# Kernel optimization log

Measured on AMD Instinct MI355X. Metric: run time of the kernel, lower is better.

## Reference

```python
import jax, jax.numpy as jnp
import numpy as np

B, K, T, C, F = 2048, 32, 365, 4, 128  # batch, prototypes, steps, bands, feature_size


def conv1d(x, w, b, pad):
    # x: (B, Cin, T), w: (Cout, Cin, Kw)
    y = jax.lax.conv_general_dilated(x, w, (1,), [(pad, pad)],
                                     dimension_numbers=('NCH', 'OIH', 'NCH'))
    return y + b[None, :, None]


def bn_relu(x, gamma, beta):
    # training-mode BatchNorm1d over (batch, time) per channel
    mu = x.mean((0, 2), keepdims=True)
    var = x.var((0, 2), keepdims=True)
    xn = (x - mu) * jax.lax.rsqrt(var + 1e-5)
    return jax.nn.relu(xn * gamma[None, :, None] + beta[None, :, None])


def encoder(x, w1, b1, g1, be1, w2, b2, g2, be2, w3, b3, g3, be3, fc_w, fc_b):
    # FCNBaseline: 3 conv blocks + global average pool + linear
    h = x.transpose(0, 2, 1)                    # (B, C, T)
    h = bn_relu(conv1d(h, w1, b1, 4), g1, be1)  # (B, 128, T+1)
    h = bn_relu(conv1d(h, w2, b2, 2), g2, be2)  # (B, 256, *)
    h = bn_relu(conv1d(h, w3, b3, 1), g3, be3)  # (B, 128, *)
    return h.mean(-1) @ fc_w.T + fc_b           # (B, F)


def setup_inputs() -> dict:
    key = jax.random.key(0)
    ks = jax.random.split(key, 12)
    input_seq = jax.random.normal(ks[0], (B, T, C), jnp.float32)
    label = jax.random.randint(ks[1], (B,), 0, 9)
    mask = (jax.random.uniform(ks[2], (B, T)) > 0.2).astype(jnp.float32)
    prototypes = jax.random.normal(ks[3], (K, T, C), jnp.float32)
    w1 = jax.random.normal(ks[4], (128, C, 8)) * 0.05
    b1 = jnp.zeros((128,)); g1 = jnp.ones((128,)); be1 = jnp.zeros((128,))
    w2 = jax.random.normal(ks[5], (256, 128, 5)) * 0.05
    b2 = jnp.zeros((256,)); g2 = jnp.ones((256,)); be2 = jnp.zeros((256,))
    w3 = jax.random.normal(ks[6], (128, 256, 3)) * 0.05
    b3 = jnp.zeros((128,)); g3 = jnp.ones((128,)); be3 = jnp.zeros((128,))
    fc_w = jax.random.normal(ks[7], (F, 128)) * 0.05
    fc_b = jnp.zeros((F,))
    off_w = jax.random.normal(ks[8], (K * C, F)) * 0.05
    off_b = jnp.zeros((K * C,))
    return dict(input_seq=input_seq, label=label, mask=mask, prototypes=prototypes,
                w1=w1, b1=b1, g1=g1, be1=be1, w2=w2, b2=b2, g2=g2, be2=be2,
                w3=w3, b3=b3, g3=g3, be3=be3, fc_w=fc_w, fc_b=fc_b,
                off_w=off_w, off_b=off_b)


def reference(input_seq, label, mask, prototypes, w1, b1, g1, be1, w2, b2, g2, be2,
              w3, b3, g3, be3, fc_w, fc_b, off_w, off_b):
    # trans_activ=False (TPS warp disabled), offset_activ=True, unsupervised path
    feat = encoder(input_seq, w1, b1, g1, be1, w2, b2, g2, be2, w3, b3, g3, be3, fc_w, fc_b)
    offset = jnp.tanh(feat @ off_w.T + off_b).reshape(-1, K, 1, C)  # (B,K,1,C)
    protos = prototypes[None] + offset                              # (B,K,T,C)
    diff = input_seq[:, None] - protos                              # (B,K,T,C)
    # masked squared-distance reduce: mask (B,T) broadcasts over (K,C)
    distances = jnp.einsum('bktc,bt->bk', diff * diff, mask)        # (B,K)
    indices = jnp.argmin(distances, axis=1)                         # (B,)
    output_seq = jnp.take_along_axis(protos, indices[:, None, None, None], axis=1)[:, 0]
    return output_seq
```

## Files before the change

### kernel.cpp

```cpp
#include <hip/hip_runtime.h>
#include <hip/hip_bf16.h>

#define BB 2048
#define TIN 365
#define TO 366
#define C1 128
#define C2 256
#define C3 128
#define FF 128

typedef __attribute__((ext_vector_type(4))) float f32x4v;
typedef __attribute__((ext_vector_type(8))) short bf16x8;

__device__ inline unsigned short f2bf(float v) {
  unsigned u = __float_as_uint(v);
  unsigned r = (u + 0x7FFF + ((u >> 16) & 1)) >> 16;
  return (unsigned short)r;
}
__device__ inline float bf2f(unsigned short b) {
  return __uint_as_float(((unsigned)b) << 16);
}

__global__ void wprep2_kernel(const float* __restrict__ w2,
                              short* __restrict__ wh, short* __restrict__ wl) {
  int n = 256 * 128 * 5;
  for (int idx = blockIdx.x * 256 + threadIdx.x; idx < n; idx += gridDim.x * 256) {
    int k = idx % 5;
    int rest = idx / 5;
    int i = rest % 128;
    int o = rest / 128;
    float v = w2[idx];
    unsigned short hb = f2bf(v);
    unsigned short lb = f2bf(v - bf2f(hb));
    size_t dst = ((((size_t)k * 4 + (i >> 5)) * 16 + (o >> 4)) * 64 +
                  ((i >> 3) & 3) * 16 + (o & 15)) * 8 + (i & 7);
    wh[dst] = (short)hb;
    wl[dst] = (short)lb;
  }
}
__global__ void wprep3_kernel(const float* __restrict__ w3,
                              short* __restrict__ wh, short* __restrict__ wl) {
  int n = 128 * 256 * 3;
  for (int idx = blockIdx.x * 256 + threadIdx.x; idx < n; idx += gridDim.x * 256) {
    int k = idx % 3;
    int rest = idx / 3;
    int i = rest % 256;
    int o = rest / 256;
    float v = w3[idx];
    unsigned short hb = f2bf(v);
    unsigned short lb = f2bf(v - bf2f(hb));
    size_t dst = ((((size_t)k * 8 + (i >> 5)) * 8 + (o >> 4)) * 64 +
                  ((i >> 3) & 3) * 16 + (o & 15)) * 8 + (i & 7);
    wh[dst] = (short)hb;
    wl[dst] = (short)lb;
  }
}

__global__ void bnparam_kernel(const double* __restrict__ sums,
                               const float* __restrict__ gamma,
                               const float* __restrict__ beta, int Cch,
                               float* __restrict__ scale, float* __restrict__ shift) {
  int i = threadIdx.x;
  if (i < Cch) {
    const double N = (double)BB * (double)TO;
    double mean = sums[i] / N;
    double var = sums[Cch + i] / N - mean * mean;
    double sc = (double)gamma[i] / sqrt(var + 1e-5);
    scale[i] = (float)sc;
    shift[i] = (float)((double)beta[i] - mean * sc);
  }
}

__global__ __launch_bounds__(256) void conv1_stats_kernel(
    const float* __restrict__ x, const float* __restrict__ w1,
    const float* __restrict__ b1, double* __restrict__ sums) {
  __shared__ float4 xs[374];
  __shared__ float ws1[4096];
  int tid = threadIdx.x;
  for (int i = tid; i < 4096; i += 256) ws1[i] = w1[i];
  __syncthreads();
  const int o = tid >> 1, half = tid & 1;
  float wr[32];
#pragma unroll
  for (int i = 0; i < 32; ++i) wr[i] = ws1[o * 32 + i];
  const float bo = b1[o];
  float s1 = 0.f, s2 = 0.f;
  for (int b = blockIdx.x * 8; b < blockIdx.x * 8 + 8; ++b) {
    __syncthreads();
    for (int u = tid; u < 374; u += 256) {
      int t_in = u - 4;
      float4 v = make_float4(0.f, 0.f, 0.f, 0.f);
      if (t_in >= 0 && t_in < TIN) v = *(const float4*)(x + ((size_t)b * TIN + t_in) * 4);
      xs[u] = v;
    }
    __syncthreads();
    for (int t = half * 183; t < half * 183 + 183; ++t) {
      float acc = bo;
#pragma unroll
      for (int k = 0; k < 8; ++k) {
        float4 xv = xs[t + k];
        acc = fmaf(wr[k], xv.x, acc);
        acc = fmaf(wr[8 + k], xv.y, acc);
        acc = fmaf(wr[16 + k], xv.z, acc);
        acc = fmaf(wr[24 + k], xv.w, acc);
      }
      s1 += acc; s2 += acc * acc;
    }
  }
  s1 += __shfl_xor(s1, 1);
  s2 += __shfl_xor(s2, 1);
  if (half == 0) {
    atomicAdd(&sums[o], (double)s1);
    atomicAdd(&sums[C1 + o], (double)s2);
  }
}

__global__ __launch_bounds__(256) void conv2_mfma_kernel(
    const float* __restrict__ x, const float* __restrict__ w1g,
    const float* __restrict__ b1, const float* __restrict__ scale1,
    const float* __restrict__ shift1, const short* __restrict__ w2ph,
    const short* __restrict__ w2pl, const float* __restrict__ b2,
    float* __restrict__ p2) {
  __shared__ float ws1[4096];
  __shared__ float4 xwin[76];
  __shared__ __align__(16) short h1h[68 * 72];
  __shared__ __align__(16) short h1l[68 * 72];
  __shared__ float sstat[512];
  const int tid = threadIdx.x;
  const int tt = blockIdx.x, b = blockIdx.y;
  const int tbase = tt * 64;
  const int slice = (b * 6 + tt) & 63;
  const int w = tid >> 6, lane = tid & 63;
  const int q = lane >> 4, l15 = lane & 15;

  for (int i = tid; i < 4096; i += 256) ws1[i] = w1g[i];
  for (int u = tid; u < 76; u += 256) {
    int tx = tbase - 6 + u;
    float4 v = make_float4(0.f, 0.f, 0.f, 0.f);
    if (tx >= 0 && tx < TIN) v = *(const float4*)(x + ((size_t)b * TIN + tx) * 4);
    xwin[u] = v;
  }
  float b2r[4][4];
#pragma unroll
  for (int om = 0; om < 4; ++om)
#pragma unroll
    for (int r = 0; r < 4; ++r) b2r[om][r] = b2[64 * w + om * 16 + q * 4 + r];

  f32x4v acc[4][4];
#pragma unroll
  for (int om = 0; om < 4; ++om)
#pragma unroll
    for (int nt = 0; nt < 4; ++nt) acc[om][nt] = (f32x4v){0.f, 0.f, 0.f, 0.f};

  const int chl = tid >> 2, qt = tid & 3;
  for (int ic2 = 0; ic2 < 2; ++ic2) {
    __syncthreads();
    {
      int ch = ic2 * 64 + chl;
      float sc = scale1[ch], sh = shift1[ch], bo = b1[ch];
      const float* wr = &ws1[ch * 32];
      for (int j = 0; j < 17; ++j) {
        int u = qt * 17 + j;
        int t = tbase - 2 + u;
        float a = bo;
#pragma unroll
        for (int kk = 0; kk < 8; ++kk) {
          float4 xv = xwin[u + kk];
          a = fmaf(wr[kk], xv.x, a);
          a = fmaf(wr[8 + kk], xv.y, a);
          a = fmaf(wr[16 + kk], xv.z, a);
          a = fmaf(wr[24 + kk], xv.w, a);
        }
        float v = (t >= 0 && t < TO) ? fmaxf(fmaf(sc, a, sh), 0.f) : 0.f;
        unsigned short hb = f2bf(v);
        h1h[u * 72 + chl] = (short)hb;
        h1l[u * 72 + chl] = (short)f2bf(v - bf2f(hb));
      }
    }
    __syncthreads();
    for (int k = 0; k < 5; ++k) {
      for (int ic = 0; ic < 2; ++ic) {
        int icg = ic2 * 2 + ic;
        bf16x8 ah[4], al[4];
#pragma unroll
        for (int om = 0; om < 4; ++om) {
          int og = 4 * w + om;
          size_t base = ((((size_t)k * 4 + icg) * 16 + og) * 64 + lane) * 8;
          ah[om] = *(const bf16x8*)(w2ph + base);
          al[om] = *(const bf16x8*)(w2pl + base);
        }
        int ioff = ic * 32 + q * 8;
#pragma unroll
        for (int nt = 0; nt < 4; ++nt) {
          int u = nt * 16 + l15 + k;
          bf16x8 bh = *(const bf16x8*)&h1h[u * 72 + ioff];
          bf16x8 bl = *(const bf16x8*)&h1l[u * 72 + ioff];
#pragma unroll
          for (int om = 0; om < 4; ++om) {
            acc[om][nt] = __builtin_amdgcn_mfma_f32_16x16x32_bf16(ah[om], bh, acc[om][nt], 0, 0, 0);
            acc[om][nt] = __builtin_amdgcn_mfma_f32_16x16x32_bf16(ah[om], bl, acc[om][nt], 0, 0, 0);
            acc[om][nt] = __builtin_amdgcn_mfma_f32_16x16x32_bf16(al[om], bh, acc[om][nt], 0, 0, 0);
          }
        }
      }
    }
  }
  float ts1[16], ts2[16];
#pragma unroll
  for (int i = 0; i < 16; ++i) { ts1[i] = 0.f; ts2[i] = 0.f; }
#pragma unroll
  for (int om = 0; om < 4; ++om)
#pragma unroll
    for (int nt = 0; nt < 4; ++nt) {
      int t = tbase + nt * 16 + l15;
      if (t < TO) {
#pragma unroll
        for (int r = 0; r < 4; ++r) {
          float v = acc[om][nt][r] + b2r[om][r];
          ts1[om * 4 + r] += v;
          ts2[om * 4 + r] += v * v;
        }
      }
    }
#pragma unroll
  for (int i = 0; i < 16; ++i) {
#pragma unroll
    for (int d = 1; d < 16; d <<= 1) {
      ts1[i] += __shfl_xor(ts1[i], d);
      ts2[i] += __shfl_xor(ts2[i], d);
    }
  }
  if (l15 == 0) {
#pragma unroll
    for (int om = 0; om < 4; ++om)
#pragma unroll
      for (int r = 0; r < 4; ++r) {
        int o = 64 * w + om * 16 + q * 4 + r;
        sstat[o] = ts1[om * 4 + r];
        sstat[256 + o] = ts2[om * 4 + r];
      }
  }
  __syncthreads();
  atomicAdd(&p2[(size_t)tid * 64 + slice], sstat[tid]);
  atomicAdd(&p2[((size_t)tid + 256) * 64 + slice], sstat[tid + 256]);
}

template <int EPI>
__global__ __launch_bounds__(256) void fused23_kernel(
    const float* __restrict__ x, const float* __restrict__ w1g,
    const float* __restrict__ b1, const float* __restrict__ scale1,
    const float* __restrict__ shift1, const short* __restrict__ w2ph,
    const short* __restrict__ w2pl, const float* __restrict__ b2,
    const float* __restrict__ scale2, const float* __restrict__ shift2,
    const short* __restrict__ w3ph, const short* __restrict__ w3pl,
    const float* __restrict__ b3, const float* __restrict__ scale3,
    const float* __restrict__ shift3, float* __restrict__ p3,
    float* __restrict__ pooled, float* __restrict__ h3g,
    int bstore, int boff) {
  __shared__ float4 xwin[80];
  __shared__ __align__(16) short un[17424];
  __shared__ float bn2s[768];
  __shared__ float sstat[256];
  short* h1h = un;
  short* h1l = un + 70 * 72;
  short* h2sh = un;
  short* h2sl = un + 66 * 132;
  const int tid = threadIdx.x;
  const int tt = blockIdx.x;
  const int b = blockIdx.y + boff;
  const int tbase = tt * 64;
  const int slice = (b * 6 + tt) & 63;
  const int w = tid >> 6, lane = tid & 63;
  const int q = lane >> 4, l15 = lane & 15;

  for (int u = tid; u < 77; u += 256) {
    int tx = tbase - 7 + u;
    float4 v = make_float4(0.f, 0.f, 0.f, 0.f);
    if (tx >= 0 && tx < TIN) v = *(const float4*)(x + ((size_t)b * TIN + tx) * 4);
    xwin[u] = v;
  }
  bn2s[tid] = b2[tid];
  bn2s[256 + tid] = scale2[tid];
  bn2s[512 + tid] = shift2[tid];

  float b3r[2][4], sc3r[2][4], sh3r[2][4];
#pragma unroll
  for (int om = 0; om < 2; ++om)
#pragma unroll
    for (int r = 0; r < 4; ++r) {
      int o = 32 * w + om * 16 + q * 4 + r;
      b3r[om][r] = b3[o];
      if (EPI == 1) { sc3r[om][r] = scale3[o]; sh3r[om][r] = shift3[o]; }
    }

  f32x4v acc2[4][5];
#pragma unroll
  for (int om = 0; om < 4; ++om)
#pragma unroll
    for (int nt = 0; nt < 5; ++nt) acc2[om][nt] = (f32x4v){0.f, 0.f, 0.f, 0.f};

  const int chl = tid >> 2, qt = tid & 3;
  for (int ic2 = 0; ic2 < 2; ++ic2) {
    int ch = ic2 * 64 + chl;
    float wr[32];
#pragma unroll
    for (int i = 0; i < 32; ++i) wr[i] = w1g[ch * 32 + i];
    float sc = scale1[ch], sh = shift1[ch], bo = b1[ch];
    __syncthreads();
    for (int j = 0; j < 18; ++j) {
      int u1 = qt * 18 + j;
      if (u1 < 70) {
        int t1 = tbase - 3 + u1;
        float a = bo;
#pragma unroll
        for (int kk = 0; kk < 8; ++kk) {
          float4 xv = xwin[u1 + kk];
          a = fmaf(wr[kk], xv.x, a);
          a = fmaf(wr[8 + kk], xv.y, a);
          a = fmaf(wr[16 + kk], xv.z, a);
          a = fmaf(wr[24 + kk], xv.w, a);
        }
        float v = (t1 >= 0 && t1 < TO) ? fmaxf(fmaf(sc, a, sh), 0.f) : 0.f;
        unsigned short hb = f2bf(v);
        h1h[u1 * 72 + chl] = (short)hb;
        h1l[u1 * 72 + chl] = (short)f2bf(v - bf2f(hb));
      }
    }
    __syncthreads();
    for (int k = 0; k < 5; ++k) {
      for (int ic = 0; ic < 2; ++ic) {
        int icg = ic2 * 2 + ic;
        bf16x8 ah[4], al[4];
#pragma unroll
        for (int om = 0; om < 4; ++om) {
          int og = 4 * w + om;
          size_t base = ((((size_t)k * 4 + icg) * 16 + og) * 64 + lane) * 8;
          ah[om] = *(const bf16x8*)(w2ph + base);
          al[om] = *(const bf16x8*)(w2pl + base);
        }
        int ioff = ic * 32 + q * 8;
#pragma unroll
        for (int nt = 0; nt < 5; ++nt) {
          int u1 = nt * 16 + l15 + k;
          if (u1 > 69) u1 = 69;
          bf16x8 bh = *(const bf16x8*)&h1h[u1 * 72 + ioff];
          bf16x8 bl = *(const bf16x8*)&h1l[u1 * 72 + ioff];
#pragma unroll
          for (int om = 0; om < 4; ++om) {
            acc2[om][nt] = __builtin_amdgcn_mfma_f32_16x16x32_bf16(ah[om], bh, acc2[om][nt], 0, 0, 0);
            acc2[om][nt] = __builtin_amdgcn_mfma_f32_16x16x32_bf16(ah[om], bl, acc2[om][nt], 0, 0, 0);
            acc2[om][nt] = __builtin_amdgcn_mfma_f32_16x16x32_bf16(al[om], bh, acc2[om][nt], 0, 0, 0);
          }
        }
      }
    }
  }
  __syncthreads();
  f32x4v acc3[2][4];
#pragma unroll
  for (int om = 0; om < 2; ++om)
#pragma unroll
    for (int nt = 0; nt < 4; ++nt) acc3[om][nt] = (f32x4v){0.f, 0.f, 0.f, 0.f};
  for (int c = 0; c < 2; ++c) {
    if (c) __syncthreads();
#pragma unroll
    for (int ml = 0; ml < 2; ++ml) {
      int om = 2 * c + ml;
      int og = 4 * w + om;
#pragma unroll
      for (int nt = 0; nt < 5; ++nt) {
        int u2 = nt * 16 + l15;
        if (u2 < 66) {
          int t2 = tbase - 1 + u2;
          bool valid = (t2 >= 0 && t2 < TO);
#pragma unroll
          for (int rp = 0; rp < 2; ++rp) {
            int o = og * 16 + q * 4 + rp * 2;
            int ol = (w * 2 + ml) * 16 + q * 4 + rp * 2;
            float v0 = 0.f, v1 = 0.f;
            if (valid) {
              v0 = fmaxf(fmaf(bn2s[256 + o], acc2[om][nt][rp * 2] + bn2s[o], bn2s[512 + o]), 0.f);
              v1 = fmaxf(fmaf(bn2s[256 + o + 1], acc2[om][nt][rp * 2 + 1] + bn2s[o + 1], bn2s[512 + o + 1]), 0.f);
            }
            unsigned short hb0 = f2bf(v0), hb1 = f2bf(v1);
            *(unsigned*)&h2sh[u2 * 132 + ol] = (unsigned)hb0 | ((unsigned)hb1 << 16);
            *(unsigned*)&h2sl[u2 * 132 + ol] =
                (unsigned)f2bf(v0 - bf2f(hb0)) | ((unsigned)f2bf(v1 - bf2f(hb1)) << 16);
          }
        }
      }
    }
    __syncthreads();
    for (int k = 0; k < 3; ++k) {
      for (int e = 0; e < 4; ++e) {
        int icg = c + 2 * e;
        bf16x8 a3h[2], a3l[2];
#pragma unroll
        for (int om = 0; om < 2; ++om) {
          int og = 2 * w + om;
          size_t base = ((((size_t)k * 8 + icg) * 8 + og) * 64 + lane) * 8;
          a3h[om] = *(const bf16x8*)(w3ph + base);
          a3l[om] = *(const bf16x8*)(w3pl + base);
        }
        int ioff = e * 32 + q * 8;
#pragma unroll
        for (int nt = 0; nt < 4; ++nt) {
          int u = nt * 16 + l15 + k;
          bf16x8 bh = *(const bf16x8*)&h2sh[u * 132 + ioff];
          bf16x8 bl = *(const bf16x8*)&h2sl[u * 132 + ioff];
#pragma unroll
          for (int om = 0; om < 2; ++om) {
            acc3[om][nt] = __builtin_amdgcn_mfma_f32_16x16x32_bf16(a3h[om], bh, acc3[om][nt], 0, 0, 0);
            acc3[om][nt] = __builtin_amdgcn_mfma_f32_16x16x32_bf16(a3l[om], bh, acc3[om][nt], 0, 0, 0);
            acc3[om][nt] = __builtin_amdgcn_mfma_f32_16x16x32_bf16(a3h[om], bl, acc3[om][nt], 0, 0, 0);
          }
        }
      }
    }
  }
  if (EPI == 0) {
    float ts1[8], ts2[8];
#pragma unroll
    for (int i = 0; i < 8; ++i) { ts1[i] = 0.f; ts2[i] = 0.f; }
    bool st = (b < bstore);
#pragma unroll
    for (int om = 0; om < 2; ++om)
#pragma unroll
      for (int nt = 0; nt < 4; ++nt) {
        int t = tbase + nt * 16 + l15;
        if (t < TO) {
#pragma unroll
          for (int r = 0; r < 4; ++r) {
            float v = acc3[om][nt][r] + b3r[om][r];
            ts1[om * 4 + r] += v;
            ts2[om * 4 + r] += v * v;
            if (st) {
              int o = 32 * w + om * 16 + q * 4 + r;
              h3g[((size_t)b * 128 + o) * 368 + t] = v;
            }
          }
        }
      }
#pragma unroll
    for (int i = 0; i < 8; ++i) {
#pragma unroll
      for (int d = 1; d < 16; d <<= 1) {
        ts1[i] += __shfl_xor(ts1[i], d);
        ts2[i] += __shfl_xor(ts2[i], d);
      }
    }
    if (l15 == 0) {
#pragma unroll
      for (int om = 0; om < 2; ++om)
#pragma unroll
        for (int r = 0; r < 4; ++r) {
          int o = 32 * w + om * 16 + q * 4 + r;
          sstat[o] = ts1[om * 4 + r];
          sstat[128 + o] = ts2[om * 4 + r];
        }
    }
    __syncthreads();
    atomicAdd(&p3[(size_t)tid * 64 + slice], sstat[tid]);
  } else {
    float ps[8];
#pragma unroll
    for (int i = 0; i < 8; ++i) ps[i] = 0.f;
#pragma unroll
    for (int om = 0; om < 2; ++om)
#pragma unroll
      for (int nt = 0; nt < 4; ++nt) {
        int t = tbase + nt * 16 + l15;
        if (t < TO) {
#pragma unroll
          for (int r = 0; r < 4; ++r) {
            float v = acc3[om][nt][r] + b3r[om][r];
            ps[om * 4 + r] += fmaxf(fmaf(sc3r[om][r], v, sh3r[om][r]), 0.f);
          }
        }
      }
#pragma unroll
    for (int i = 0; i < 8; ++i) {
#pragma unroll
      for (int d = 1; d < 16; d <<= 1) ps[i] += __shfl_xor(ps[i], d);
    }
    if (l15 == 0) {
#pragma unroll
      for (int om = 0; om < 2; ++om)
#pragma unroll
        for (int r = 0; r < 4; ++r) {
          int o = 32 * w + om * 16 + q * 4 + r;
          atomicAdd(&pooled[(size_t)b * 128 + o], ps[om * 4 + r]);
        }
    }
  }
}

__global__ __launch_bounds__(256) void gap3_kernel(
    const float* __restrict__ h3g, const float* __restrict__ scale3,
    const float* __restrict__ shift3, float* __restrict__ pooled) {
  int b = blockIdx.x, tid = threadIdx.x;
  int w = tid >> 6, lane = tid & 63;
  for (int cc = 0; cc < 32; ++cc) {
    int ch = w * 32 + cc;
    float sc = scale3[ch], sh = shift3[ch];
    const float* row = h3g + ((size_t)b * 128 + ch) * 368;
    float s = 0.f;
    for (int u = lane; u < TO; u += 64)
      s += fmaxf(fmaf(sc, row[u], sh), 0.f);
#pragma unroll
    for (int d = 32; d > 0; d >>= 1) s += __shfl_xor(s, d);
    if (lane == 0) pooled[(size_t)b * 128 + ch] = s;
  }
}

__global__ __launch_bounds__(64) void reduce_slices_kernel(
    const float* __restrict__ p, double* __restrict__ sums) {
  int c = blockIdx.x, tid = threadIdx.x;
  double s = (double)p[(size_t)c * 64 + tid];
  for (int d = 32; d > 0; d >>= 1) s += __shfl_down(s, d);
  if (tid == 0) sums[c] = s;
}

__global__ __launch_bounds__(128) void head2_kernel(
    const float* __restrict__ pooled, const float* __restrict__ fc_w,
    const float* __restrict__ fc_b, const float* __restrict__ off_w,
    const float* __restrict__ off_b, float* __restrict__ offs) {
  int b = blockIdx.x, tid = threadIdx.x;
  __shared__ float pl[128], feat[128];
  pl[tid] = pooled[(size_t)b * C3 + tid] * (1.0f / 366.0f);
  __syncthreads();
  {
    const float* wr = fc_w + tid * FF;
    float a = fc_b[tid];
    for (int i = 0; i < 128; ++i) a = fmaf(pl[i], wr[i], a);
    feat[tid] = a;
  }
  __syncthreads();
  {
    const float* wr = off_w + tid * FF;
    float z = off_b[tid];
    for (int i = 0; i < 128; ++i) z = fmaf(feat[i], wr[i], z);
    offs[(size_t)b * 128 + tid] = tanhf(z);
  }
}

__global__ __launch_bounds__(256) void dist_kernel(
    const float* __restrict__ x, const float* __restrict__ mask,
    const float* __restrict__ protos, const float* __restrict__ offs,
    float* __restrict__ out) {
  int b = blockIdx.x, tid = threadIdx.x;
  __shared__ float ofl[128];
  __shared__ double dred[256];
  __shared__ int ksel;
  if (tid < 128) ofl[tid] = offs[(size_t)b * 128 + tid];
  __syncthreads();
  int k = tid & 31, tg = tid >> 5;
  float o0 = ofl[k * 4 + 0], o1 = ofl[k * 4 + 1], o2 = ofl[k * 4 + 2], o3 = ofl[k * 4 + 3];
  double acc = 0.0;
  for (int t = tg; t < TIN; t += 8) {
    float4 xv = *(const float4*)(x + ((size_t)b * TIN + t) * 4);
    float4 pv = *(const float4*)(protos + ((size_t)k * TIN + t) * 4);
    float m = mask[(size_t)b * TIN + t];
    float d0 = xv.x - pv.x - o0;
    float d1 = xv.y - pv.y - o1;
    float d2 = xv.z - pv.z - o2;
    float d3 = xv.w - pv.w - o3;
    acc += (double)(m * (d0 * d0 + d1 * d1 + d2 * d2 + d3 * d3));
  }
  dred[tid] = acc;
  __syncthreads();
  if (tid < 32) {
    double s = 0.0;
    for (int g = 0; g < 8; ++g) s += dred[g * 32 + tid];
    dred[tid] = s;
  }
  __syncthreads();
  if (tid == 0) {
    double best = dred[0]; int bi = 0;
    for (int kk = 1; kk < 32; ++kk)
      if (dred[kk] < best) { best = dred[kk]; bi = kk; }
    ksel = bi;
  }
  __syncthreads();
  int km = ksel;
  const float* psrc = protos + (size_t)km * TIN * 4;
  float* dst = out + (size_t)b * TIN * 4;
  for (int u = tid; u < TIN * 4; u += 256)
    dst[u] = psrc[u] + ofl[km * 4 + (u & 3)];
}

extern "C" void kernel_launch(void* const* d_in, const int* in_sizes, int n_in,
                              void* d_out, int out_size, void* d_ws, size_t ws_size,
                              hipStream_t stream) {
  const float* x      = (const float*)d_in[0];
  const float* mask   = (const float*)d_in[2];
  const float* protos = (const float*)d_in[3];
  const float* w1 = (const float*)d_in[4];
  const float* b1 = (const float*)d_in[5];
  const float* g1 = (const float*)d_in[6];
  const float* be1 = (const float*)d_in[7];
  const float* w2 = (const float*)d_in[8];
  const float* b2 = (const float*)d_in[9];
  const float* g2 = (const float*)d_in[10];
  const float* be2 = (const float*)d_in[11];
  const float* w3 = (const float*)d_in[12];
  const float* b3 = (const float*)d_in[13];
  const float* g3 = (const float*)d_in[14];
  const float* be3 = (const float*)d_in[15];
  const float* fc_w = (const float*)d_in[16];
  const float* fc_b = (const float*)d_in[17];
  const float* off_w = (const float*)d_in[18];
  const float* off_b = (const float*)d_in[19];
  float* out = (float*)d_out;
  (void)in_sizes; (void)n_in; (void)out_size;

  char* wsp = (char*)d_ws;
  size_t off = 0;
  auto alloc = [&](size_t bytes) { void* p = wsp + off; off += (bytes + 255) & ~(size_t)255; return p; };
  float* bnp   = (float*)alloc(1024 * 4);
  float* offs  = (float*)alloc((size_t)BB * 128 * 4);
  size_t zero_beg = off;
  double* sums  = (double*)alloc(1024 * 8);
  float* pooled = (float*)alloc((size_t)BB * C3 * 4);
  float* p2     = (float*)alloc((size_t)512 * 64 * 4);
  float* p3     = (float*)alloc((size_t)256 * 64 * 4);
  size_t zero_end = off;
  short* w2ph = (short*)alloc((size_t)256 * 128 * 5 * 2);
  short* w2pl = (short*)alloc((size_t)256 * 128 * 5 * 2);
  short* w3ph = (short*)alloc((size_t)128 * 256 * 3 * 2);
  short* w3pl = (short*)alloc((size_t)128 * 256 * 3 * 2);
  size_t small_end = off;
  float* h3g = (float*)(wsp + small_end);
  int bstore = 0;
  if (ws_size > small_end) {
    size_t cap = (ws_size - small_end) / ((size_t)128 * 368 * 4);
    bstore = (int)(cap > (size_t)BB ? (size_t)BB : cap);
  }

  double* sums1 = sums;
  double* sums2 = sums + 256;
  double* sums3 = sums + 768;
  float* scale1 = bnp;        float* shift1 = bnp + 128;
  float* scale2 = bnp + 256;  float* shift2 = bnp + 512;
  float* scale3 = bnp + 768;  float* shift3 = bnp + 896;

  hipMemsetAsync(wsp + zero_beg, 0, zero_end - zero_beg, stream);

  conv1_stats_kernel<<<256, 256, 0, stream>>>(x, w1, b1, sums1);
  bnparam_kernel<<<1, 256, 0, stream>>>(sums1, g1, be1, C1, scale1, shift1);

  wprep2_kernel<<<256, 256, 0, stream>>>(w2, w2ph, w2pl);
  wprep3_kernel<<<128, 256, 0, stream>>>(w3, w3ph, w3pl);

  conv2_mfma_kernel<<<dim3(6, BB), 256, 0, stream>>>(
      x, w1, b1, scale1, shift1, w2ph, w2pl, b2, p2);
  reduce_slices_kernel<<<512, 64, 0, stream>>>(p2, sums2);
  bnparam_kernel<<<1, 256, 0, stream>>>(sums2, g2, be2, C2, scale2, shift2);

  fused23_kernel<0><<<dim3(6, BB), 256, 0, stream>>>(
      x, w1, b1, scale1, shift1, w2ph, w2pl, b2, scale2, shift2,
      w3ph, w3pl, b3, scale3, shift3, p3, pooled, h3g, bstore, 0);
  reduce_slices_kernel<<<256, 64, 0, stream>>>(p3, sums3);
  bnparam_kernel<<<1, 256, 0, stream>>>(sums3, g3, be3, C3, scale3, shift3);

  if (bstore > 0)
    gap3_kernel<<<bstore, 256, 0, stream>>>(h3g, scale3, shift3, pooled);
  if (bstore < BB)
    fused23_kernel<1><<<dim3(6, BB - bstore), 256, 0, stream>>>(
        x, w1, b1, scale1, shift1, w2ph, w2pl, b2, scale2, shift2,
        w3ph, w3pl, b3, scale3, shift3, p3, pooled, h3g, 0, bstore);

  head2_kernel<<<BB, 128, 0, stream>>>(pooled, fc_w, fc_b, off_w, off_b, offs);
  dist_kernel<<<BB, 256, 0, stream>>>(x, mask, protos, offs, out);
}
```

Measured before the change: 4.501 ms.

## Drop h3 workspace caching and keep conv1 weights in registers

```diff
diff --git a/kernel.cpp b/kernel.cpp
--- a/kernel.cpp
+++ b/kernel.cpp
@@ -121,7 +121,6 @@
     const float* __restrict__ shift1, const short* __restrict__ w2ph,
     const short* __restrict__ w2pl, const float* __restrict__ b2,
     float* __restrict__ p2) {
-  __shared__ float ws1[4096];
   __shared__ float4 xwin[76];
   __shared__ __align__(16) short h1h[68 * 72];
   __shared__ __align__(16) short h1l[68 * 72];
@@ -133,7 +132,6 @@
   const int w = tid >> 6, lane = tid & 63;
   const int q = lane >> 4, l15 = lane & 15;
 
-  for (int i = tid; i < 4096; i += 256) ws1[i] = w1g[i];
   for (int u = tid; u < 76; u += 256) {
     int tx = tbase - 6 + u;
     float4 v = make_float4(0.f, 0.f, 0.f, 0.f);
@@ -154,28 +152,28 @@
 
   const int chl = tid >> 2, qt = tid & 3;
   for (int ic2 = 0; ic2 < 2; ++ic2) {
-    __syncthreads();
-    {
-      int ch = ic2 * 64 + chl;
-      float sc = scale1[ch], sh = shift1[ch], bo = b1[ch];
-      const float* wr = &ws1[ch * 32];
-      for (int j = 0; j < 17; ++j) {
-        int u = qt * 17 + j;
-        int t = tbase - 2 + u;
-        float a = bo;
-#pragma unroll
-        for (int kk = 0; kk < 8; ++kk) {
-          float4 xv = xwin[u + kk];
-          a = fmaf(wr[kk], xv.x, a);
-          a = fmaf(wr[8 + kk], xv.y, a);
-          a = fmaf(wr[16 + kk], xv.z, a);
-          a = fmaf(wr[24 + kk], xv.w, a);
-        }
-        float v = (t >= 0 && t < TO) ? fmaxf(fmaf(sc, a, sh), 0.f) : 0.f;
-        unsigned short hb = f2bf(v);
-        h1h[u * 72 + chl] = (short)hb;
-        h1l[u * 72 + chl] = (short)f2bf(v - bf2f(hb));
-      }
+    int ch = ic2 * 64 + chl;
+    float wr[32];
+#pragma unroll
+    for (int i = 0; i < 32; ++i) wr[i] = w1g[ch * 32 + i];
+    float sc = scale1[ch], sh = shift1[ch], bo = b1[ch];
+    __syncthreads();
+    for (int j = 0; j < 17; ++j) {
+      int u = qt * 17 + j;
+      int t = tbase - 2 + u;
+      float a = bo;
+#pragma unroll
+      for (int kk = 0; kk < 8; ++kk) {
+        float4 xv = xwin[u + kk];
+        a = fmaf(wr[kk], xv.x, a);
+        a = fmaf(wr[8 + kk], xv.y, a);
+        a = fmaf(wr[16 + kk], xv.z, a);
+        a = fmaf(wr[24 + kk], xv.w, a);
+      }
+      float v = (t >= 0 && t < TO) ? fmaxf(fmaf(sc, a, sh), 0.f) : 0.f;
+      unsigned short hb = f2bf(v);
+      h1h[u * 72 + chl] = (short)hb;
+      h1l[u * 72 + chl] = (short)f2bf(v - bf2f(hb));
     }
     __syncthreads();
     for (int k = 0; k < 5; ++k) {
@@ -255,8 +253,7 @@
     const short* __restrict__ w3ph, const short* __restrict__ w3pl,
     const float* __restrict__ b3, const float* __restrict__ scale3,
     const float* __restrict__ shift3, float* __restrict__ p3,
-    float* __restrict__ pooled, float* __restrict__ h3g,
-    int bstore, int boff) {
+    float* __restrict__ pooled) {
   __shared__ float4 xwin[80];
   __shared__ __align__(16) short un[17424];
   __shared__ float bn2s[768];
@@ -267,7 +264,7 @@
   short* h2sl = un + 66 * 132;
   const int tid = threadIdx.x;
   const int tt = blockIdx.x;
-  const int b = blockIdx.y + boff;
+  const int b = blockIdx.y;
   const int tbase = tt * 64;
   const int slice = (b * 6 + tt) & 63;
   const int w = tid >> 6, lane = tid & 63;
@@ -422,7 +419,6 @@
     float ts1[8], ts2[8];
 #pragma unroll
     for (int i = 0; i < 8; ++i) { ts1[i] = 0.f; ts2[i] = 0.f; }
-    bool st = (b < bstore);
 #pragma unroll
     for (int om = 0; om < 2; ++om)
 #pragma unroll
@@ -434,10 +430,6 @@
             float v = acc3[om][nt][r] + b3r[om][r];
             ts1[om * 4 + r] += v;
             ts2[om * 4 + r] += v * v;
-            if (st) {
-              int o = 32 * w + om * 16 + q * 4 + r;
-              h3g[((size_t)b * 128 + o) * 368 + t] = v;
-            }
           }
         }
       }
@@ -492,24 +484,6 @@
           atomicAdd(&pooled[(size_t)b * 128 + o], ps[om * 4 + r]);
         }
     }
-  }
-}
-
-__global__ __launch_bounds__(256) void gap3_kernel(
-    const float* __restrict__ h3g, const float* __restrict__ scale3,
-    const float* __restrict__ shift3, float* __restrict__ pooled) {
-  int b = blockIdx.x, tid = threadIdx.x;
-  int w = tid >> 6, lane = tid & 63;
-  for (int cc = 0; cc < 32; ++cc) {
-    int ch = w * 32 + cc;
-    float sc = scale3[ch], sh = shift3[ch];
-    const float* row = h3g + ((size_t)b * 128 + ch) * 368;
-    float s = 0.f;
-    for (int u = lane; u < TO; u += 64)
-      s += fmaxf(fmaf(sc, row[u], sh), 0.f);
-#pragma unroll
-    for (int d = 32; d > 0; d >>= 1) s += __shfl_xor(s, d);
-    if (lane == 0) pooled[(size_t)b * 128 + ch] = s;
   }
 }
 
@@ -612,7 +586,7 @@
   const float* off_w = (const float*)d_in[18];
   const float* off_b = (const float*)d_in[19];
   float* out = (float*)d_out;
-  (void)in_sizes; (void)n_in; (void)out_size;
+  (void)in_sizes; (void)n_in; (void)out_size; (void)ws_size;
 
   char* wsp = (char*)d_ws;
   size_t off = 0;
@@ -629,13 +603,6 @@
   short* w2pl = (short*)alloc((size_t)256 * 128 * 5 * 2);
   short* w3ph = (short*)alloc((size_t)128 * 256 * 3 * 2);
   short* w3pl = (short*)alloc((size_t)128 * 256 * 3 * 2);
-  size_t small_end = off;
-  float* h3g = (float*)(wsp + small_end);
-  int bstore = 0;
-  if (ws_size > small_end) {
-    size_t cap = (ws_size - small_end) / ((size_t)128 * 368 * 4);
-    bstore = (int)(cap > (size_t)BB ? (size_t)BB : cap);
-  }
 
   double* sums1 = sums;
   double* sums2 = sums + 256;
@@ -659,16 +626,13 @@
 
   fused23_kernel<0><<<dim3(6, BB), 256, 0, stream>>>(
       x, w1, b1, scale1, shift1, w2ph, w2pl, b2, scale2, shift2,
-      w3ph, w3pl, b3, scale3, shift3, p3, pooled, h3g, bstore, 0);
+      w3ph, w3pl, b3, scale3, shift3, p3, pooled);
   reduce_slices_kernel<<<256, 64, 0, stream>>>(p3, sums3);
   bnparam_kernel<<<1, 256, 0, stream>>>(sums3, g3, be3, C3, scale3, shift3);
 
-  if (bstore > 0)
-    gap3_kernel<<<bstore, 256, 0, stream>>>(h3g, scale3, shift3, pooled);
-  if (bstore < BB)
-    fused23_kernel<1><<<dim3(6, BB - bstore), 256, 0, stream>>>(
-        x, w1, b1, scale1, shift1, w2ph, w2pl, b2, scale2, shift2,
-        w3ph, w3pl, b3, scale3, shift3, p3, pooled, h3g, 0, bstore);
+  fused23_kernel<1><<<dim3(6, BB), 256, 0, stream>>>(
+      x, w1, b1, scale1, shift1, w2ph, w2pl, b2, scale2, shift2,
+      w3ph, w3pl, b3, scale3, shift3, p3, pooled);
 
   head2_kernel<<<BB, 128, 0, stream>>>(pooled, fc_w, fc_b, off_w, off_b, offs);
   dist_kernel<<<BB, 256, 0, stream>>>(x, mask, protos, offs, out);
```

After: 5.731 ms. 1.27x slower.
